# Optimization experiments

Measured on AMD Instinct MI355X. Metric: run time of the kernel, lower is better.

The kernel has to match this reference:

```python
import jax, jax.numpy as jnp
import numpy as np

F_, E_, B_, D_, H_, O_ = 4, 8, 4096, 512, 1024, 512


def setup_inputs() -> dict:
    key = jax.random.key(0)
    ks = jax.random.split(key, 7)
    s = 0.02  # small init scale to keep activations sane
    return {
        "features": jax.random.normal(ks[0], (F_, B_, D_), jnp.float32),
        "W1": jax.random.normal(ks[1], (F_, E_, D_, H_), jnp.float32) * s,
        "b1": jax.random.normal(ks[2], (F_, E_, H_), jnp.float32) * s,
        "W2": jax.random.normal(ks[3], (F_, E_, H_, O_), jnp.float32) * s,
        "b2": jax.random.normal(ks[4], (F_, E_, O_), jnp.float32) * s,
        "Wg": jax.random.normal(ks[5], (F_, D_, E_), jnp.float32) * s,
        "bg": jax.random.normal(ks[6], (F_, E_), jnp.float32) * s,
    }


def reference(features, W1, b1, W2, b2, Wg, bg):
    # Gate: softmax over experts, per feature. [F,B,E]
    gate = jax.nn.softmax(jnp.einsum('fbd,fde->fbe', features, Wg) + bg[:, None, :], axis=-1)
    # All experts computed densely (soft MoE): hidden [F,B,E,H]
    h = jax.nn.relu(jnp.einsum('fbd,fedh->fbeh', features, W1) + b1[:, None, :, :])
    # Expert outputs [F,B,E,O]
    eo = jnp.einsum('fbeh,feho->fbeo', h, W2) + b2[:, None, :, :]
    # Gate-weighted sum over experts, then mean over features -> [B,O]
    weighted = jnp.einsum('fbe,fbeo->fbo', gate, eo)
    return jnp.mean(weighted, axis=0)
```

## Files before the change

kernel.cpp:

```cpp
#include <hip/hip_runtime.h>


#define F_ 4
#define E_ 8
#define B_ 4096
#define D_ 512
#define H_ 1024
#define O_ 512

typedef unsigned short ushort_t;
typedef __bf16 bf16x8 __attribute__((ext_vector_type(8)));
typedef float f32x4 __attribute__((ext_vector_type(4)));

__device__ inline ushort_t f2bf(float f) {
  union { float f; unsigned u; } v; v.f = f;
  unsigned r = v.u + 0x7FFFu + ((v.u >> 16) & 1u);
  return (ushort_t)(r >> 16);
}

__device__ inline void async16(const void* g, void* l) {
  __builtin_amdgcn_global_load_lds(
      (const __attribute__((address_space(1))) unsigned int*)g,
      (__attribute__((address_space(3))) unsigned int*)l, 16, 0, 0);
}

__global__ void cast_feat_kernel(const float* __restrict__ in, ushort_t* __restrict__ out) {
  const int i = blockIdx.x * 256 + threadIdx.x;
  const float4 v = ((const float4*)in)[i];
  ushort4 o;
  o.x = f2bf(v.x); o.y = f2bf(v.y); o.z = f2bf(v.z); o.w = f2bf(v.w);
  ((ushort4*)out)[i] = o;
}

__global__ void transpose_cast_kernel(const float* __restrict__ in, ushort_t* __restrict__ out,
                                      int R, int C) {
  __shared__ float tile[64][65];
  const size_t zoff = (size_t)blockIdx.z * R * C;
  in += zoff; out += zoff;
  const int tx = threadIdx.x & 63, ty = threadIdx.x >> 6;
  const int r0 = blockIdx.y * 64, c0 = blockIdx.x * 64;
#pragma unroll
  for (int i = 0; i < 16; ++i) {
    const int r = ty + i * 4;
    tile[r][tx] = in[(size_t)(r0 + r) * C + c0 + tx];
  }
  __syncthreads();
#pragma unroll
  for (int i = 0; i < 16; ++i) {
    const int c = ty + i * 4;
    out[(size_t)(c0 + c) * R + r0 + tx] = f2bf(tile[tx][c]);
  }
}

__global__ void gate_kernel(const float* __restrict__ features, const float* __restrict__ Wg,
                            const float* __restrict__ bg, float* __restrict__ g2) {
  const int fb = blockIdx.x;
  const int f = fb >> 12, b = fb & (B_ - 1);
  const int lane = threadIdx.x;
  const float* feat = features + ((size_t)f * B_ + b) * D_;
  const float* wg = Wg + (size_t)f * D_ * E_;
  float acc[E_] = {0.f, 0.f, 0.f, 0.f, 0.f, 0.f, 0.f, 0.f};
  for (int d = lane; d < D_; d += 64) {
    const float fv = feat[d];
    const float4 w0 = ((const float4*)(wg + d * E_))[0];
    const float4 w1 = ((const float4*)(wg + d * E_))[1];
    acc[0] += fv * w0.x; acc[1] += fv * w0.y; acc[2] += fv * w0.z; acc[3] += fv * w0.w;
    acc[4] += fv * w1.x; acc[5] += fv * w1.y; acc[6] += fv * w1.z; acc[7] += fv * w1.w;
  }
#pragma unroll
  for (int off = 32; off >= 1; off >>= 1)
#pragma unroll
    for (int e = 0; e < E_; ++e) acc[e] += __shfl_xor(acc[e], off, 64);
  float lg[E_], mx = -1e30f;
#pragma unroll
  for (int e = 0; e < E_; ++e) { lg[e] = acc[e] + bg[f * E_ + e]; mx = fmaxf(mx, lg[e]); }
  float s = 0.f;
#pragma unroll
  for (int e = 0; e < E_; ++e) { lg[e] = __expf(lg[e] - mx); s += lg[e]; }
  const float inv = 1.f / (s * (float)F_);
  if (lane < E_) g2[((size_t)f * B_ + b) * E_ + lane] = lg[lane] * inv;
}

__global__ __launch_bounds__(256, 3) void gemm1_kernel(
    const ushort_t* __restrict__ A, const ushort_t* __restrict__ Bt,
    const float* __restrict__ b1, const float* __restrict__ g2,
    ushort_t* __restrict__ Hf) {
  __shared__ ushort_t As[128 * 32];
  __shared__ ushort_t Bs[128 * 32];
  const int id = blockIdx.x;
  const int e = id & 7;
  const int s = id >> 3;
  const int n0 = (s & 7) * 128;
  const int m0 = (s >> 3) * 128;
  const ushort_t* Bp = Bt + (size_t)e * H_ * D_;

  const int t = threadIdx.x, lane = t & 63, w = t >> 6;
  const int wm = w & 1, wn = w >> 1;
  const int lr = lane & 15, q = lane >> 4;
  const int pc = q ^ ((lr >> 1) & 3);

  const int r0 = t >> 2;
  const int g = (t & 3) ^ ((r0 >> 1) & 3);
  const char* aSrc0 = (const char*)A + (size_t)(m0 + r0) * (D_ * 2) + g * 16;
  const char* aSrc1 = (const char*)A + (size_t)(m0 + r0 + 64) * (D_ * 2) + g * 16;
  const char* bSrc0 = (const char*)Bp + (size_t)(n0 + r0) * (D_ * 2) + g * 16;
  const char* bSrc1 = (const char*)Bp + (size_t)(n0 + r0 + 64) * (D_ * 2) + g * 16;
  ushort_t* aDst0 = &As[t * 8];  ushort_t* aDst1 = &As[2048 + t * 8];
  ushort_t* bDst0 = &Bs[t * 8];  ushort_t* bDst1 = &Bs[2048 + t * 8];

  f32x4 acc[4][4];
#pragma unroll
  for (int i = 0; i < 4; ++i)
#pragma unroll
    for (int j = 0; j < 4; ++j) acc[i][j] = (f32x4){0.f, 0.f, 0.f, 0.f};

  for (int ks = 0; ks < D_ / 32; ++ks) {
    async16(aSrc0, aDst0); async16(aSrc1, aDst1);
    async16(bSrc0, bDst0); async16(bSrc1, bDst1);
    aSrc0 += 64; aSrc1 += 64; bSrc0 += 64; bSrc1 += 64;
    __syncthreads();
    bf16x8 af[4], bfr[4];
#pragma unroll
    for (int i = 0; i < 4; ++i)
      af[i] = *(const bf16x8*)&As[(wm * 64 + i * 16 + lr) * 32 + pc * 8];
#pragma unroll
    for (int j = 0; j < 4; ++j)
      bfr[j] = *(const bf16x8*)&Bs[(wn * 64 + j * 16 + lr) * 32 + pc * 8];
#pragma unroll
    for (int i = 0; i < 4; ++i)
#pragma unroll
      for (int j = 0; j < 4; ++j)
        acc[i][j] = __builtin_amdgcn_mfma_f32_16x16x32_bf16(af[i], bfr[j], acc[i][j], 0, 0, 0);
    __syncthreads();
  }

  const float* b1e = b1 + (size_t)e * H_;
#pragma unroll
  for (int i = 0; i < 4; ++i) {
#pragma unroll
    for (int r = 0; r < 4; ++r) {
      const int m = m0 + wm * 64 + i * 16 + q * 4 + r;
      const float gv = g2[m * E_ + e];
#pragma unroll
      for (int j = 0; j < 4; ++j) {
        const int n = n0 + wn * 64 + j * 16 + lr;
        float v = acc[i][j][r] + b1e[n];
        v = fmaxf(v, 0.f) * gv;
        Hf[((size_t)e * B_ + m) * H_ + n] = f2bf(v);
      }
    }
  }
}

__global__ __launch_bounds__(256, 3) void gemm2_kernel(
    const ushort_t* __restrict__ Hf, const ushort_t* __restrict__ Bt,
    const float* __restrict__ b2, const float* __restrict__ g2,
    float* __restrict__ part, float* __restrict__ out) {
  __shared__ ushort_t As[128 * 32];
  __shared__ ushort_t Bs[128 * 32];
  const int id = blockIdx.x;
  const int e = id & 7;
  const int s = id >> 3;
  const int n0 = (s & 3) * 128;
  const int m0 = (s >> 2) * 128;
  const ushort_t* Ap = Hf + (size_t)e * B_ * H_;
  const ushort_t* Bp = Bt + (size_t)e * O_ * H_;

  const int t = threadIdx.x, lane = t & 63, w = t >> 6;
  const int wm = w & 1, wn = w >> 1;
  const int lr = lane & 15, q = lane >> 4;
  const int pc = q ^ ((lr >> 1) & 3);

  const int r0 = t >> 2;
  const int g = (t & 3) ^ ((r0 >> 1) & 3);
  const char* aSrc0 = (const char*)Ap + (size_t)(m0 + r0) * (H_ * 2) + g * 16;
  const char* aSrc1 = (const char*)Ap + (size_t)(m0 + r0 + 64) * (H_ * 2) + g * 16;
  const char* bSrc0 = (const char*)Bp + (size_t)(n0 + r0) * (H_ * 2) + g * 16;
  const char* bSrc1 = (const char*)Bp + (size_t)(n0 + r0 + 64) * (H_ * 2) + g * 16;
  ushort_t* aDst0 = &As[t * 8];  ushort_t* aDst1 = &As[2048 + t * 8];
  ushort_t* bDst0 = &Bs[t * 8];  ushort_t* bDst1 = &Bs[2048 + t * 8];

  f32x4 acc[4][4];
#pragma unroll
  for (int i = 0; i < 4; ++i)
#pragma unroll
    for (int j = 0; j < 4; ++j) acc[i][j] = (f32x4){0.f, 0.f, 0.f, 0.f};

  for (int ks = 0; ks < H_ / 32; ++ks) {
    async16(aSrc0, aDst0); async16(aSrc1, aDst1);
    async16(bSrc0, bDst0); async16(bSrc1, bDst1);
    aSrc0 += 64; aSrc1 += 64; bSrc0 += 64; bSrc1 += 64;
    __syncthreads();
    bf16x8 af[4], bfr[4];
#pragma unroll
    for (int i = 0; i < 4; ++i)
      af[i] = *(const bf16x8*)&As[(wm * 64 + i * 16 + lr) * 32 + pc * 8];
#pragma unroll
    for (int j = 0; j < 4; ++j)
      bfr[j] = *(const bf16x8*)&Bs[(wn * 64 + j * 16 + lr) * 32 + pc * 8];
#pragma unroll
    for (int i = 0; i < 4; ++i)
#pragma unroll
      for (int j = 0; j < 4; ++j)
        acc[i][j] = __builtin_amdgcn_mfma_f32_16x16x32_bf16(af[i], bfr[j], acc[i][j], 0, 0, 0);
    __syncthreads();
  }

  const float* b2e = b2 + (size_t)e * O_;
#pragma unroll
  for (int i = 0; i < 4; ++i) {
#pragma unroll
    for (int r = 0; r < 4; ++r) {
      const int m = m0 + wm * 64 + i * 16 + q * 4 + r;
      const float gv = g2[m * E_ + e];
#pragma unroll
      for (int j = 0; j < 4; ++j) {
        const int n = n0 + wn * 64 + j * 16 + lr;
        const float v = acc[i][j][r] + gv * b2e[n];
        if (part) part[((size_t)e * B_ + m) * O_ + n] = v;
        else atomicAdd(&out[(size_t)m * O_ + n], v);
      }
    }
  }
}

__global__ void reduce_kernel(const float4* __restrict__ part, float4* __restrict__ out) {
  const int p = blockIdx.x * 256 + threadIdx.x;
  float4 s = part[p];
#pragma unroll
  for (int e = 1; e < E_; ++e) {
    const float4 v = part[(size_t)e * (B_ * O_ / 4) + p];
    s.x += v.x; s.y += v.y; s.z += v.z; s.w += v.w;
  }
  float4 o = out[p];
  o.x += s.x; o.y += s.y; o.z += s.z; o.w += s.w;
  out[p] = o;
}

extern "C" void kernel_launch(void* const* d_in, const int* in_sizes, int n_in,
                              void* d_out, int out_size, void* d_ws, size_t ws_size,
                              hipStream_t stream) {
  const float* features = (const float*)d_in[0];
  const float* W1 = (const float*)d_in[1];
  const float* b1 = (const float*)d_in[2];
  const float* W2 = (const float*)d_in[3];
  const float* b2 = (const float*)d_in[4];
  const float* Wg = (const float*)d_in[5];
  const float* bg = (const float*)d_in[6];
  float* out = (float*)d_out;

  char* ws = (char*)d_ws;
  ushort_t* featbf = (ushort_t*)ws;
  ushort_t* w1t    = (ushort_t*)(ws + 16777216);
  ushort_t* w2t    = (ushort_t*)(ws + 50331648);
  float*    g2     = (float*)(ws + 83886080);
  ushort_t* Hf     = (ushort_t*)(ws + 84410368);
  float*    part   = (float*)(ws + 151519232);
  const bool big = ws_size >= (size_t)218628096;
  float* partArg = big ? part : nullptr;

  cast_feat_kernel<<<F_ * B_ * D_ / 1024, 256, 0, stream>>>(features, featbf);
  transpose_cast_kernel<<<dim3(H_ / 64, D_ / 64, F_ * E_), 256, 0, stream>>>(W1, w1t, D_, H_);
  transpose_cast_kernel<<<dim3(O_ / 64, H_ / 64, F_ * E_), 256, 0, stream>>>(W2, w2t, H_, O_);
  gate_kernel<<<F_ * B_, 64, 0, stream>>>(features, Wg, bg, g2);
  hipMemsetAsync(d_out, 0, (size_t)B_ * O_ * sizeof(float), stream);

  for (int f = 0; f < F_; ++f) {
    gemm1_kernel<<<(B_ / 128) * (H_ / 128) * E_, 256, 0, stream>>>(
        featbf + (size_t)f * B_ * D_,
        w1t + (size_t)f * E_ * H_ * D_,
        b1 + (size_t)f * E_ * H_,
        g2 + (size_t)f * B_ * E_,
        Hf);
    gemm2_kernel<<<(B_ / 128) * (O_ / 128) * E_, 256, 0, stream>>>(
        Hf,
        w2t + (size_t)f * E_ * O_ * H_,
        b2 + (size_t)f * E_ * O_,
        g2 + (size_t)f * B_ * E_,
        partArg, out);
    if (big)
      reduce_kernel<<<B_ * O_ / 4 / 256, 256, 0, stream>>>((const float4*)part, (float4*)out);
  }
}
```

Baseline: 669.7 us.

## Stage GEMM epilogues through LDS, merge expert pairs, store bf16 partials, reduce once

The GEMM1 and GEMM2 epilogues now write through a padded LDS tile and issue 16-byte coalesced global stores instead of scattered 2-byte stores. GEMM2 accumulates two experts per block, which halves the number of partial outputs. Partials are kept in bf16 and reduced by a single final kernel over all 16 slices instead of one reduction per feature. This removes the memset, cuts partial-buffer traffic and kernel launches, but rounding partial sums to bf16 adds precision error.

```diff
diff --git a/kernel.cpp b/kernel.cpp
--- a/kernel.cpp
+++ b/kernel.cpp
@@ -11,11 +11,16 @@
 typedef unsigned short ushort_t;
 typedef __bf16 bf16x8 __attribute__((ext_vector_type(8)));
 typedef float f32x4 __attribute__((ext_vector_type(4)));
+typedef unsigned short ushort8_t __attribute__((ext_vector_type(8)));
 
 __device__ inline ushort_t f2bf(float f) {
   union { float f; unsigned u; } v; v.f = f;
   unsigned r = v.u + 0x7FFFu + ((v.u >> 16) & 1u);
   return (ushort_t)(r >> 16);
+}
+__device__ inline float bf2f(ushort_t u) {
+  union { unsigned u; float f; } v; v.u = ((unsigned)u) << 16;
+  return v.f;
 }
 
 __device__ inline void async16(const void* g, void* l) {
@@ -81,12 +86,15 @@
   if (lane < E_) g2[((size_t)f * B_ + b) * E_ + lane] = lg[lane] * inv;
 }
 
+#define EPI_STRIDE 136
+
 __global__ __launch_bounds__(256, 3) void gemm1_kernel(
     const ushort_t* __restrict__ A, const ushort_t* __restrict__ Bt,
     const float* __restrict__ b1, const float* __restrict__ g2,
     ushort_t* __restrict__ Hf) {
-  __shared__ ushort_t As[128 * 32];
-  __shared__ ushort_t Bs[128 * 32];
+  __shared__ __align__(16) ushort_t smem[128 * EPI_STRIDE];
+  ushort_t* As = smem;
+  ushort_t* Bs = smem + 4096;
   const int id = blockIdx.x;
   const int e = id & 7;
   const int s = id >> 3;
@@ -139,32 +147,39 @@
   for (int i = 0; i < 4; ++i) {
 #pragma unroll
     for (int r = 0; r < 4; ++r) {
-      const int m = m0 + wm * 64 + i * 16 + q * 4 + r;
-      const float gv = g2[m * E_ + e];
+      const int ml = wm * 64 + i * 16 + q * 4 + r;
+      const float gv = g2[(m0 + ml) * E_ + e];
 #pragma unroll
       for (int j = 0; j < 4; ++j) {
-        const int n = n0 + wn * 64 + j * 16 + lr;
-        float v = acc[i][j][r] + b1e[n];
+        const int nl = wn * 64 + j * 16 + lr;
+        float v = acc[i][j][r] + b1e[n0 + nl];
         v = fmaxf(v, 0.f) * gv;
-        Hf[((size_t)e * B_ + m) * H_ + n] = f2bf(v);
+        smem[ml * EPI_STRIDE + nl] = f2bf(v);
       }
     }
   }
+  __syncthreads();
+  const int row = t >> 1, half = t & 1;
+  const ushort_t* src = &smem[row * EPI_STRIDE + half * 64];
+  ushort_t* dst = Hf + ((size_t)e * B_ + m0 + row) * H_ + n0 + half * 64;
+#pragma unroll
+  for (int c = 0; c < 8; ++c)
+    *(ushort8_t*)(dst + c * 8) = *(const ushort8_t*)(src + c * 8);
 }
 
 __global__ __launch_bounds__(256, 3) void gemm2_kernel(
     const ushort_t* __restrict__ Hf, const ushort_t* __restrict__ Bt,
     const float* __restrict__ b2, const float* __restrict__ g2,
-    float* __restrict__ part, float* __restrict__ out) {
-  __shared__ ushort_t As[128 * 32];
-  __shared__ ushort_t Bs[128 * 32];
+    ushort_t* __restrict__ part) {
+  __shared__ __align__(16) ushort_t smem[128 * EPI_STRIDE];
+  ushort_t* As = smem;
+  ushort_t* Bs = smem + 4096;
   const int id = blockIdx.x;
-  const int e = id & 7;
-  const int s = id >> 3;
+  const int grp = id & 3;
+  const int s = id >> 2;
   const int n0 = (s & 3) * 128;
   const int m0 = (s >> 2) * 128;
-  const ushort_t* Ap = Hf + (size_t)e * B_ * H_;
-  const ushort_t* Bp = Bt + (size_t)e * O_ * H_;
+  const int e0 = grp * 2;
 
   const int t = threadIdx.x, lane = t & 63, w = t >> 6;
   const int wm = w & 1, wn = w >> 1;
@@ -173,10 +188,6 @@
 
   const int r0 = t >> 2;
   const int g = (t & 3) ^ ((r0 >> 1) & 3);
-  const char* aSrc0 = (const char*)Ap + (size_t)(m0 + r0) * (H_ * 2) + g * 16;
-  const char* aSrc1 = (const char*)Ap + (size_t)(m0 + r0 + 64) * (H_ * 2) + g * 16;
-  const char* bSrc0 = (const char*)Bp + (size_t)(n0 + r0) * (H_ * 2) + g * 16;
-  const char* bSrc1 = (const char*)Bp + (size_t)(n0 + r0 + 64) * (H_ * 2) + g * 16;
   ushort_t* aDst0 = &As[t * 8];  ushort_t* aDst1 = &As[2048 + t * 8];
   ushort_t* bDst0 = &Bs[t * 8];  ushort_t* bDst1 = &Bs[2048 + t * 8];
 
@@ -186,55 +197,74 @@
 #pragma unroll
     for (int j = 0; j < 4; ++j) acc[i][j] = (f32x4){0.f, 0.f, 0.f, 0.f};
 
-  for (int ks = 0; ks < H_ / 32; ++ks) {
-    async16(aSrc0, aDst0); async16(aSrc1, aDst1);
-    async16(bSrc0, bDst0); async16(bSrc1, bDst1);
-    aSrc0 += 64; aSrc1 += 64; bSrc0 += 64; bSrc1 += 64;
-    __syncthreads();
-    bf16x8 af[4], bfr[4];
-#pragma unroll
-    for (int i = 0; i < 4; ++i)
-      af[i] = *(const bf16x8*)&As[(wm * 64 + i * 16 + lr) * 32 + pc * 8];
-#pragma unroll
-    for (int j = 0; j < 4; ++j)
-      bfr[j] = *(const bf16x8*)&Bs[(wn * 64 + j * 16 + lr) * 32 + pc * 8];
-#pragma unroll
-    for (int i = 0; i < 4; ++i)
+  for (int h = 0; h < 2; ++h) {
+    const int e = e0 + h;
+    const ushort_t* Ap = Hf + (size_t)e * B_ * H_;
+    const ushort_t* Bp = Bt + (size_t)e * O_ * H_;
+    const char* aSrc0 = (const char*)Ap + (size_t)(m0 + r0) * (H_ * 2) + g * 16;
+    const char* aSrc1 = (const char*)Ap + (size_t)(m0 + r0 + 64) * (H_ * 2) + g * 16;
+    const char* bSrc0 = (const char*)Bp + (size_t)(n0 + r0) * (H_ * 2) + g * 16;
+    const char* bSrc1 = (const char*)Bp + (size_t)(n0 + r0 + 64) * (H_ * 2) + g * 16;
+    for (int ks = 0; ks < H_ / 32; ++ks) {
+      async16(aSrc0, aDst0); async16(aSrc1, aDst1);
+      async16(bSrc0, bDst0); async16(bSrc1, bDst1);
+      aSrc0 += 64; aSrc1 += 64; bSrc0 += 64; bSrc1 += 64;
+      __syncthreads();
+      bf16x8 af[4], bfr[4];
+#pragma unroll
+      for (int i = 0; i < 4; ++i)
+        af[i] = *(const bf16x8*)&As[(wm * 64 + i * 16 + lr) * 32 + pc * 8];
 #pragma unroll
       for (int j = 0; j < 4; ++j)
-        acc[i][j] = __builtin_amdgcn_mfma_f32_16x16x32_bf16(af[i], bfr[j], acc[i][j], 0, 0, 0);
-    __syncthreads();
-  }
-
-  const float* b2e = b2 + (size_t)e * O_;
+        bfr[j] = *(const bf16x8*)&Bs[(wn * 64 + j * 16 + lr) * 32 + pc * 8];
+#pragma unroll
+      for (int i = 0; i < 4; ++i)
+#pragma unroll
+        for (int j = 0; j < 4; ++j)
+          acc[i][j] = __builtin_amdgcn_mfma_f32_16x16x32_bf16(af[i], bfr[j], acc[i][j], 0, 0, 0);
+      __syncthreads();
+    }
+  }
+
+  const float* b2e0 = b2 + (size_t)e0 * O_;
+  const float* b2e1 = b2e0 + O_;
 #pragma unroll
   for (int i = 0; i < 4; ++i) {
 #pragma unroll
     for (int r = 0; r < 4; ++r) {
-      const int m = m0 + wm * 64 + i * 16 + q * 4 + r;
-      const float gv = g2[m * E_ + e];
+      const int ml = wm * 64 + i * 16 + q * 4 + r;
+      const float gv0 = g2[(m0 + ml) * E_ + e0];
+      const float gv1 = g2[(m0 + ml) * E_ + e0 + 1];
 #pragma unroll
       for (int j = 0; j < 4; ++j) {
-        const int n = n0 + wn * 64 + j * 16 + lr;
-        const float v = acc[i][j][r] + gv * b2e[n];
-        if (part) part[((size_t)e * B_ + m) * O_ + n] = v;
-        else atomicAdd(&out[(size_t)m * O_ + n], v);
+        const int nl = wn * 64 + j * 16 + lr;
+        const int n = n0 + nl;
+        const float v = acc[i][j][r] + gv0 * b2e0[n] + gv1 * b2e1[n];
+        smem[ml * EPI_STRIDE + nl] = f2bf(v);
       }
     }
   }
-}
-
-__global__ void reduce_kernel(const float4* __restrict__ part, float4* __restrict__ out) {
-  const int p = blockIdx.x * 256 + threadIdx.x;
-  float4 s = part[p];
-#pragma unroll
-  for (int e = 1; e < E_; ++e) {
-    const float4 v = part[(size_t)e * (B_ * O_ / 4) + p];
-    s.x += v.x; s.y += v.y; s.z += v.z; s.w += v.w;
-  }
-  float4 o = out[p];
-  o.x += s.x; o.y += s.y; o.z += s.z; o.w += s.w;
-  out[p] = o;
+  __syncthreads();
+  const int row = t >> 1, half = t & 1;
+  const ushort_t* src = &smem[row * EPI_STRIDE + half * 64];
+  ushort_t* dst = part + (size_t)grp * (B_ * O_) + ((size_t)(m0 + row)) * O_ + n0 + half * 64;
+#pragma unroll
+  for (int c = 0; c < 8; ++c)
+    *(ushort8_t*)(dst + c * 8) = *(const ushort8_t*)(src + c * 8);
+}
+
+__global__ void reduce_kernel(const ushort_t* __restrict__ part, float* __restrict__ out) {
+  const size_t p = ((size_t)blockIdx.x * 256 + threadIdx.x) * 8;
+  float s[8] = {0.f, 0.f, 0.f, 0.f, 0.f, 0.f, 0.f, 0.f};
+#pragma unroll
+  for (int k = 0; k < F_ * 4; ++k) {
+    const ushort8_t u = *(const ushort8_t*)&part[(size_t)k * (B_ * O_) + p];
+#pragma unroll
+    for (int j = 0; j < 8; ++j) s[j] += bf2f(u[j]);
+  }
+  float4 o0 = {s[0], s[1], s[2], s[3]}, o1 = {s[4], s[5], s[6], s[7]};
+  *(float4*)&out[p] = o0;
+  *(float4*)&out[p + 4] = o1;
 }
 
 extern "C" void kernel_launch(void* const* d_in, const int* in_sizes, int n_in,
@@ -255,15 +285,12 @@
   ushort_t* w2t    = (ushort_t*)(ws + 50331648);
   float*    g2     = (float*)(ws + 83886080);
   ushort_t* Hf     = (ushort_t*)(ws + 84410368);
-  float*    part   = (float*)(ws + 151519232);
-  const bool big = ws_size >= (size_t)218628096;
-  float* partArg = big ? part : nullptr;
+  ushort_t* part   = (ushort_t*)(ws + 151519232);
 
   cast_feat_kernel<<<F_ * B_ * D_ / 1024, 256, 0, stream>>>(features, featbf);
   transpose_cast_kernel<<<dim3(H_ / 64, D_ / 64, F_ * E_), 256, 0, stream>>>(W1, w1t, D_, H_);
   transpose_cast_kernel<<<dim3(O_ / 64, H_ / 64, F_ * E_), 256, 0, stream>>>(W2, w2t, H_, O_);
   gate_kernel<<<F_ * B_, 64, 0, stream>>>(features, Wg, bg, g2);
-  hipMemsetAsync(d_out, 0, (size_t)B_ * O_ * sizeof(float), stream);
 
   for (int f = 0; f < F_; ++f) {
     gemm1_kernel<<<(B_ / 128) * (H_ / 128) * E_, 256, 0, stream>>>(
@@ -272,13 +299,12 @@
         b1 + (size_t)f * E_ * H_,
         g2 + (size_t)f * B_ * E_,
         Hf);
-    gemm2_kernel<<<(B_ / 128) * (O_ / 128) * E_, 256, 0, stream>>>(
+    gemm2_kernel<<<(B_ / 128) * (O_ / 128) * 4, 256, 0, stream>>>(
         Hf,
         w2t + (size_t)f * E_ * O_ * H_,
         b2 + (size_t)f * E_ * O_,
         g2 + (size_t)f * B_ * E_,
-        partArg, out);
-    if (big)
-      reduce_kernel<<<B_ * O_ / 4 / 256, 256, 0, stream>>>((const float4*)part, (float4*)out);
-  }
-}
+        part + (size_t)f * 4 * B_ * O_);
+  }
+  reduce_kernel<<<B_ * O_ / 8 / 256, 256, 0, stream>>>(part, out);
+}
```

Result: no change. 669.2 us (-0.1%).
